# Optimization experiments

Hardware: AMD Instinct MI355X
Metric: run time of the kernel (lower is better)

## Reference

```python
import jax, jax.numpy as jnp
import numpy as np
from jax import lax

THETA = 1.0      # neuron['theta']
TAU_SR = 10.0    # neuron['tauSr'] (SRM synaptic time constant)
TAU_RHO = 1.0    # surrogate-gradient width
SCALE_RHO = 1.0  # surrogate-gradient scale
T_SIM = 100      # simulation['tSample']


def srm_kernel(T, dtype=jnp.float32):
    t = jnp.arange(T, dtype=dtype)
    return (t / TAU_SR) * jnp.exp(1.0 - t / TAU_SR)  # eps(0)=0, peak 1 at t=tau


def psp(x, eps):
    """Causal temporal filter along last axis: y[t] = sum_k eps[k] * x[t-k]."""
    shape = x.shape
    T = shape[-1]
    xf = x.reshape(-1, 1, T)
    k = eps[::-1].reshape(1, 1, T)
    y = lax.conv_general_dilated(xf, k, (1,), [(T - 1, 0)],
                                 dimension_numbers=('NCH', 'OIH', 'NCH'))
    return y.reshape(shape)


def spike(u):
    return (u >= THETA).astype(u.dtype)


def conv_t(x, w, pad):
    """Per-timestep 2D conv. x:[B,C,H,W,T], w:[O,I,kh,kw] -> [B,O,H',W',T]."""
    B, C, H, W, T = x.shape
    xt = jnp.moveaxis(x, -1, 1).reshape(B * T, C, H, W)
    y = lax.conv_general_dilated(xt, w, (1, 1), [(pad, pad), (pad, pad)],
                                 dimension_numbers=('NCHW', 'OIHW', 'NCHW'))
    O, Ho, Wo = y.shape[1], y.shape[2], y.shape[3]
    return jnp.moveaxis(y.reshape(B, T, O, Ho, Wo), 1, -1)


def pool2(x):
    """SLAYER pool: 2x2 sum with fixed weight 1.1. x:[B,C,H,W,T]."""
    B, C, H, W, T = x.shape
    xr = x.reshape(B, C, H // 2, 2, W // 2, 2, T)
    return 1.1 * xr.sum(axis=(3, 5))


def dense_t(x, w):
    """x:[B,C,H,W,T] flattened over CHW; w:[O, C*H*W] -> [B,O,T]."""
    B = x.shape[0]
    T = x.shape[-1]
    xf = x.reshape(B, -1, T)
    return jnp.einsum('bit,oi->bot', xf, w)


def setup_inputs() -> dict:
    key = jax.random.key(0)
    k = jax.random.split(key, 6)
    img = jax.random.uniform(k[0], (32, 1, 28, 28), dtype=jnp.float32)
    rand_u = jax.random.uniform(k[1], (32, 1, 28, 28, T_SIM), dtype=jnp.float32)
    w1 = jax.random.normal(k[2], (16, 1, 5, 5), dtype=jnp.float32) * 0.2
    w2 = jax.random.normal(k[3], (32, 16, 5, 5), dtype=jnp.float32) * 0.05
    wf1 = jax.random.normal(k[4], (410, 1568), dtype=jnp.float32) * 0.05
    wf2 = jax.random.normal(k[5], (10, 410), dtype=jnp.float32) * 0.05
    return {"img": img, "rand_u": rand_u, "w1": w1, "w2": w2, "wf1": wf1, "wf2": wf2}


def reference(img, rand_u, w1, w2, wf1, wf2):
    eps = srm_kernel(T_SIM, img.dtype)
    # rate encoding: Bernoulli spikes with p = pixel intensity
    x = (rand_u < img[..., None]).astype(img.dtype)          # [B,1,28,28,T]
    x = spike(psp(conv_t(x, w1, 2), eps))                    # [B,16,28,28,T]
    x = spike(psp(pool2(x), eps))                            # [B,16,14,14,T]
    x = spike(psp(conv_t(x, w2, 2), eps))                    # [B,32,14,14,T]
    x = spike(psp(pool2(x), eps))                            # [B,32,7,7,T]
    x = spike(psp(dense_t(x, wf1), eps))                     # [B,410,T]
    x = spike(psp(jnp.einsum('bit,oi->bot', x, wf2), eps))   # [B,10,T]
    return x
```

## Files before the change

### kernel.cpp

```cpp
#include <hip/hip_runtime.h>


namespace {
constexpr int B = 32, T = 100;
constexpr double A1 = 0.90483741803595957;
constexpr double CE = 0.27182818284590452;
constexpr double SC39 = 549755813888.0;
constexpr double INV39 = 1.0 / 549755813888.0;

constexpr size_t OFF_M1 = 0;
constexpr size_t OFF_M2 = OFF_M1 + (size_t)B * T * 28 * 4;
constexpr size_t OFF_S4 = OFF_M2 + (size_t)B * T * 224 * 4;
constexpr size_t OFF_D5 = OFF_S4 + (size_t)B * T * 1568;
constexpr size_t OFF_S5 = OFF_D5 + (size_t)B * T * 410 * 8;
constexpr size_t OFF_D6 = OFF_S5 + (size_t)B * T * 410;
constexpr size_t OFF_BP = OFF_D6 + (size_t)B * T * 10 * 8;
constexpr size_t OFF_AP = OFF_D5;
}

using i32x4 = __attribute__((ext_vector_type(4))) int;
using i32x16 = __attribute__((ext_vector_type(16))) int;

__global__ void k_encode_pack(const float* __restrict__ img, const float* __restrict__ ru,
                              unsigned int* __restrict__ m1) {
  int i = blockIdx.x * 256 + threadIdx.x;
  if (i >= B * 28 * T) return;
  int t = i % T;
  int y = (i / T) % 28;
  int b = i / (T * 28);
  unsigned int m = 0;
  const float* rb = ru + ((size_t)b * 784 + y * 28) * T + t;
  const float* ib = img + b * 784 + y * 28;
  for (int x = 0; x < 28; x++) {
    m |= (rb[(size_t)x * T] < ib[x]) ? (1u << x) : 0u;
  }
  m1[((size_t)b * T + t) * 28 + y] = m;
}

__global__ __launch_bounds__(256) void k_conv1(const unsigned int* __restrict__ m1,
                                               const float* __restrict__ w1,
                                               unsigned int* __restrict__ m2) {
  __shared__ double lut[160];
  __shared__ unsigned int mrow[2][32];
  __shared__ unsigned char spk[784];
  __shared__ unsigned char spkP[2][196];
  int o = blockIdx.x % 16, b = blockIdx.x / 16;
  int tid = threadIdx.x;
  if (tid < 160) {
    int dy = tid / 32, f = tid % 32;
    double v = 0.0;
    const float* wb = w1 + o * 25 + dy * 5;
#pragma unroll
    for (int dx = 0; dx < 5; dx++)
      if ((f >> dx) & 1) v += (double)wb[dx];
    lut[tid] = v;
  }
  if (tid < 32) {
    mrow[0][tid] = 0;
    mrow[1][tid] = 0;
  }
  int y = tid / 7, xg = tid % 7;
  int py = tid / 14, px = tid % 14;
  bool act = tid < 196;
  double g1[4] = {0, 0, 0, 0}, g2[4] = {0, 0, 0, 0};
  double p1 = 0.0, p2 = 0.0;
  const unsigned int* m1b = m1 + (size_t)b * T * 28;
  if (tid < 28) mrow[0][tid + 2] = m1b[tid] << 2;
  __syncthreads();
  for (int t = 0; t < T; t++) {
    int cur = t & 1, nxt = cur ^ 1;
    bool dold = (tid < 28) && (t + 1 < T);
    unsigned int ldv = 0;
    if (dold) ldv = m1b[(t + 1) * 28 + tid] << 2;
    if (act) {
      double s0 = 0, s1 = 0, s2 = 0, s3 = 0;
      int xb = xg * 4;
      const unsigned int* mc = mrow[cur];
#pragma unroll
      for (int dy = 0; dy < 5; dy++) {
        unsigned int m = mc[y + dy];
        const double* ld = lut + dy * 32;
        s0 += ld[(m >> (xb + 0)) & 31];
        s1 += ld[(m >> (xb + 1)) & 31];
        s2 += ld[(m >> (xb + 2)) & 31];
        s3 += ld[(m >> (xb + 3)) & 31];
      }
      g1[0] = s0 + A1 * g1[0]; g2[0] = g1[0] + A1 * g2[0];
      g1[1] = s1 + A1 * g1[1]; g2[1] = g1[1] + A1 * g2[1];
      g1[2] = s2 + A1 * g1[2]; g2[2] = g1[2] + A1 * g2[2];
      g1[3] = s3 + A1 * g1[3]; g2[3] = g1[3] + A1 * g2[3];
      unsigned char* sp = spk + y * 28 + xb;
      sp[0] = (CE * (g2[0] - g1[0]) >= 1.0) ? 1 : 0;
      sp[1] = (CE * (g2[1] - g1[1]) >= 1.0) ? 1 : 0;
      sp[2] = (CE * (g2[2] - g1[2]) >= 1.0) ? 1 : 0;
      sp[3] = (CE * (g2[3] - g1[3]) >= 1.0) ? 1 : 0;
    }
    if (dold) mrow[nxt][tid + 2] = ldv;
    __syncthreads();
    if (act) {
      const unsigned char* r0 = spk + (2 * py) * 28 + 2 * px;
      int sum = (int)r0[0] + (int)r0[1] + (int)r0[28] + (int)r0[29];
      double s = 1.1 * (double)sum;
      p1 = s + A1 * p1;
      p2 = p1 + A1 * p2;
      spkP[cur][tid] = (CE * (p2 - p1) >= 1.0) ? 1 : 0;
    }
    if (tid < 14 && t > 0) {
      unsigned int m = 0;
      const unsigned char* rp = spkP[nxt] + tid * 14;
#pragma unroll
      for (int xx = 0; xx < 14; xx++) m |= ((unsigned int)rp[xx]) << xx;
      m2[((size_t)(b * T + (t - 1)) * 16 + o) * 14 + tid] = m;
    }
    __syncthreads();
  }
  if (tid < 14) {
    unsigned int m = 0;
    const unsigned char* rp = spkP[(T - 1) & 1] + tid * 14;
#pragma unroll
    for (int xx = 0; xx < 14; xx++) m |= ((unsigned int)rp[xx]) << xx;
    m2[((size_t)(b * T + (T - 1)) * 16 + o) * 14 + tid] = m;
  }
}

__global__ void k_limbs(const float* __restrict__ w2, signed char* __restrict__ AP) {
  int i = blockIdx.x * 256 + threadIdx.x;
  if (i >= 32 * 80 * 8) return;
  int dx = i & 7;
  int g = (i >> 3) % 80;
  int o = i / 640;
  int c = g >> 2, r = g & 3, eh = r >> 1, kh = r & 1;
  int lane = kh * 32 + o, e = eh * 8 + dx;
  int ci = g / 5, dy = g % 5;
  float wv = (dx < 5) ? w2[((o * 16 + ci) * 5 + dy) * 5 + dx] : 0.0f;
  long long m = llrint((double)wv * SC39);
#pragma unroll
  for (int j = 0; j < 5; j++) {
    int d = (int)((m + 128) & 255) - 128;
    AP[(size_t)((j * 20 + c) * 64 + lane) * 16 + e] = (signed char)d;
    m = (m - d) >> 8;
  }
}

__global__ __launch_bounds__(256, 1) void k_conv2t(const unsigned int* __restrict__ m2,
                                                   const signed char* __restrict__ AP,
                                                   unsigned char* __restrict__ s4) {
  __shared__ unsigned int maskW[2][2][176];
  __shared__ double part[2][2][32][30];
  __shared__ unsigned char spk[2][32][28];
  int yp = blockIdx.x % 7, b = blockIdx.x / 7;
  int y0 = yp * 2;
  int tid = threadIdx.x;
  int w = tid >> 6, l = tid & 63;
  int tp = w >> 1, kg = w & 1;
  int col = l & 31, kh = l >> 5;
  int x = col % 14;
  unsigned int wmask = (col < 28) ? 31u : 0u;
  int half = (col >= 14) ? 1 : 0;
  const unsigned int* m2b = m2 + (size_t)b * T * 224;

  const i32x4* APv = (const i32x4*)AP;
  i32x4 Af[5][10];
#pragma unroll
  for (int j = 0; j < 5; j++)
#pragma unroll
    for (int cl = 0; cl < 10; cl++)
      Af[j][cl] = APv[(size_t)((j * 20) + kg * 10 + cl) * 64 + l];

  double cg1[4] = {0, 0, 0, 0}, cg2[4] = {0, 0, 0, 0};
  double q1 = 0.0, q2 = 0.0;
  int to = tid / 7, pg = tid % 7;
  bool chainAct = tid < 224;

  auto stage = [&](int buf, int baseT) {
    if (w < 2) {
      int tS = baseT + w;
#pragma unroll
      for (int pass = 0; pass < 3; pass++) {
        if (pass == 2 && l >= 32) break;
        int e = pass * 64 + l;
        int H = e / 80, g = e % 80;
        int ci = g / 5, dy = g % 5;
        int iy = y0 - 2 + H + dy;
        unsigned int v = 0;
        if (iy >= 0 && iy < 14 && tS < T) v = m2b[(size_t)tS * 224 + ci * 14 + iy] << 2;
        maskW[buf][w][H * 80 + (g & 1) * 40 + 2 * (g >> 2) + ((g >> 1) & 1)] = v;
      }
    }
  };

  stage(0, 0);
  __syncthreads();

  for (int grp = 0; grp < 50; grp++) {
    int cur = grp & 1, nxt = cur ^ 1;

    {
      const uint4* mwv = (const uint4*)&maskW[cur][tp][0];
      int base4 = half * 20 + kh * 10 + 5 * kg;
      uint4 mk0 = mwv[base4 + 0], mk1 = mwv[base4 + 1], mk2 = mwv[base4 + 2];
      uint4 mk3 = mwv[base4 + 3], mk4 = mwv[base4 + 4];
      i32x16 ac0, ac1, ac2, ac3, ac4;
#pragma unroll
      for (int r = 0; r < 16; r++) { ac0[r] = 0; ac1[r] = 0; ac2[r] = 0; ac3[r] = 0; ac4[r] = 0; }
#pragma unroll
      for (int cl = 0; cl < 10; cl++) {
        uint4 mkv = (cl < 2) ? mk0 : (cl < 4) ? mk1 : (cl < 6) ? mk2 : (cl < 8) ? mk3 : mk4;
        unsigned int ra = (cl & 1) ? mkv.z : mkv.x;
        unsigned int rb = (cl & 1) ? mkv.w : mkv.y;
        unsigned int a5 = (ra >> x) & wmask;
        unsigned int b5 = (rb >> x) & wmask;
        i32x4 bb;
        bb[0] = (int)(((a5 & 15u) * 0x204081u) & 0x01010101u);
        bb[1] = (int)((a5 >> 4) & 1u);
        bb[2] = (int)(((b5 & 15u) * 0x204081u) & 0x01010101u);
        bb[3] = (int)((b5 >> 4) & 1u);
        ac0 = __builtin_amdgcn_mfma_i32_32x32x32_i8(Af[0][cl], bb, ac0, 0, 0, 0);
        ac1 = __builtin_amdgcn_mfma_i32_32x32x32_i8(Af[1][cl], bb, ac1, 0, 0, 0);
        ac2 = __builtin_amdgcn_mfma_i32_32x32x32_i8(Af[2][cl], bb, ac2, 0, 0, 0);
        ac3 = __builtin_amdgcn_mfma_i32_32x32x32_i8(Af[3][cl], bb, ac3, 0, 0, 0);
        ac4 = __builtin_amdgcn_mfma_i32_32x32x32_i8(Af[4][cl], bb, ac4, 0, 0, 0);
      }
      if (col < 28) {
#pragma unroll
        for (int r = 0; r < 16; r++) {
          int R = (r & 3) + 8 * (r >> 2) + 4 * kh;
          int c01 = ac1[r] * 256 + ac0[r];
          int c23 = ac3[r] * 256 + ac2[r];
          double S = ((double)ac4[r] * 65536.0 + (double)c23) * 65536.0 + (double)c01;
          part[tp][kg][R][col] = S;
        }
      }
    }

    stage(nxt, (grp + 1) * 2);
    __syncthreads();

    if (chainAct) {
#pragma unroll
      for (int g = 0; g < 2; g++) {
        const double* pa = &part[g][0][to][pg * 4];
        const double* pb = &part[g][1][to][pg * 4];
        double s0 = (pa[0] + pb[0]) * INV39;
        double s1 = (pa[1] + pb[1]) * INV39;
        double s2 = (pa[2] + pb[2]) * INV39;
        double s3 = (pa[3] + pb[3]) * INV39;
        cg1[0] = s0 + A1 * cg1[0]; cg2[0] = cg1[0] + A1 * cg2[0];
        cg1[1] = s1 + A1 * cg1[1]; cg2[1] = cg1[1] + A1 * cg2[1];
        cg1[2] = s2 + A1 * cg1[2]; cg2[2] = cg1[2] + A1 * cg2[2];
        cg1[3] = s3 + A1 * cg1[3]; cg2[3] = cg1[3] + A1 * cg2[3];
        unsigned int pk = (CE * (cg2[0] - cg1[0]) >= 1.0 ? 1u : 0u)
                        | ((CE * (cg2[1] - cg1[1]) >= 1.0 ? 1u : 0u) << 8)
                        | ((CE * (cg2[2] - cg1[2]) >= 1.0 ? 1u : 0u) << 16)
                        | ((CE * (cg2[3] - cg1[3]) >= 1.0 ? 1u : 0u) << 24);
        *(unsigned int*)&spk[g][to][pg * 4] = pk;
      }
    }
    __syncthreads();

    if (chainAct) {
      int po = to, pp = pg;
#pragma unroll
      for (int g = 0; g < 2; g++) {
        const unsigned char* sr = &spk[g][po][0];
        int sum = (int)sr[2 * pp] + (int)sr[2 * pp + 1] + (int)sr[14 + 2 * pp] + (int)sr[15 + 2 * pp];
        double s = 1.1 * (double)sum;
        q1 = s + A1 * q1;
        q2 = q1 + A1 * q2;
        s4[(size_t)(b * T + grp * 2 + g) * 1568 + po * 49 + yp * 7 + pp] =
            (CE * (q2 - q1) >= 1.0) ? 1 : 0;
      }
    }
  }
}

__global__ void k_limbs2(const float* __restrict__ wf1, signed char* __restrict__ BP) {
  int i = blockIdx.x * 256 + threadIdx.x;
  if (i >= 13 * 5 * 49 * 64) return;
  int lane = i & 63;
  int fi = i >> 6;
  int c = fi % 49;
  int j = (fi / 49) % 5;
  int ot = fi / 245;
  int o = ot * 32 + (lane & 31);
  int kb = 32 * c + (lane >> 5) * 16;
  int wd[4] = {0, 0, 0, 0};
#pragma unroll
  for (int e = 0; e < 16; e++) {
    float wv = (o < 410) ? wf1[(size_t)o * 1568 + kb + e] : 0.0f;
    long long m = llrint((double)wv * SC39);
    int d = 0;
    for (int jj = 0; jj <= j; jj++) {
      d = (int)((m + 128) & 255) - 128;
      m = (m - d) >> 8;
    }
    wd[e >> 2] |= (d & 255) << ((e & 3) * 8);
  }
  i32x4 v;
  v[0] = wd[0]; v[1] = wd[1]; v[2] = wd[2]; v[3] = wd[3];
  *(i32x4*)(BP + (size_t)i * 16) = v;
}

__global__ __launch_bounds__(256) void k_dense1m(const unsigned char* __restrict__ s4,
                                                 const signed char* __restrict__ BP,
                                                 double* __restrict__ d5) {
  int ot = blockIdx.y;
  int w = threadIdx.x >> 6, l = threadIdx.x & 63;
  int col = l & 31, kh = l >> 5;
  int btTile = blockIdx.x * 4 + w;
  const unsigned char* arow = s4 + (size_t)(btTile * 32 + col) * 1568 + kh * 16;
  const i32x4* bpv = (const i32x4*)BP + (size_t)ot * 245 * 64 + l;
  i32x16 acc0, acc1, acc2, acc3, acc4;
#pragma unroll
  for (int r = 0; r < 16; r++) {
    acc0[r] = 0; acc1[r] = 0; acc2[r] = 0; acc3[r] = 0; acc4[r] = 0;
  }
  for (int c = 0; c < 49; c++) {
    i32x4 a = *(const i32x4*)(arow + 32 * c);
    i32x4 b0 = bpv[(0 * 49 + c) * 64];
    i32x4 b1 = bpv[(1 * 49 + c) * 64];
    i32x4 b2 = bpv[(2 * 49 + c) * 64];
    i32x4 b3 = bpv[(3 * 49 + c) * 64];
    i32x4 b4 = bpv[(4 * 49 + c) * 64];
    acc0 = __builtin_amdgcn_mfma_i32_32x32x32_i8(a, b0, acc0, 0, 0, 0);
    acc1 = __builtin_amdgcn_mfma_i32_32x32x32_i8(a, b1, acc1, 0, 0, 0);
    acc2 = __builtin_amdgcn_mfma_i32_32x32x32_i8(a, b2, acc2, 0, 0, 0);
    acc3 = __builtin_amdgcn_mfma_i32_32x32x32_i8(a, b3, acc3, 0, 0, 0);
    acc4 = __builtin_amdgcn_mfma_i32_32x32x32_i8(a, b4, acc4, 0, 0, 0);
  }
  int o = ot * 32 + col;
  if (o < 410) {
#pragma unroll
    for (int r = 0; r < 16; r++) {
      int R = (r & 3) + 8 * (r >> 2) + 4 * kh;
      double v = ((((double)acc4[r] * 256.0 + (double)acc3[r]) * 256.0 +
                   (double)acc2[r]) * 256.0 + (double)acc1[r]) * 256.0 + (double)acc0[r];
      d5[(size_t)(btTile * 32 + R) * 410 + o] = v * INV39;
    }
  }
}

__global__ void k_psp5(const double* __restrict__ d5, unsigned char* __restrict__ s5) {
  int tid = blockIdx.x * 256 + threadIdx.x;
  if (tid >= B * 410) return;
  int o = tid % 410, b = tid / 410;
  double g1 = 0.0, g2 = 0.0;
  for (int t = 0; t < T; t++) {
    double s = d5[(size_t)(b * T + t) * 410 + o];
    g1 = s + A1 * g1;
    g2 = g1 + A1 * g2;
    s5[(size_t)(b * T + t) * 410 + o] = (CE * (g2 - g1) >= 1.0) ? 1 : 0;
  }
}

__global__ void k_dense2(const unsigned char* __restrict__ s5, const float* __restrict__ wf2,
                         double* __restrict__ d6) {
  int tid = blockIdx.x * 256 + threadIdx.x;
  if (tid >= B * T * 10) return;
  int o = tid % 10, bt = tid / 10;
  const unsigned char* sr = s5 + (size_t)bt * 410;
  const float* wr = wf2 + o * 410;
  double s = 0.0;
  for (int i = 0; i < 410; i++) s += (double)wr[i] * (double)sr[i];
  d6[tid] = s;
}

__global__ void k_psp6(const double* __restrict__ d6, float* __restrict__ out) {
  int tid = blockIdx.x * 256 + threadIdx.x;
  if (tid >= B * 10) return;
  int o = tid % 10, b = tid / 10;
  double g1 = 0.0, g2 = 0.0;
  for (int t = 0; t < T; t++) {
    double s = d6[(size_t)(b * T + t) * 10 + o];
    g1 = s + A1 * g1;
    g2 = g1 + A1 * g2;
    out[(size_t)b * 1000 + o * 100 + t] = (CE * (g2 - g1) >= 1.0) ? 1.0f : 0.0f;
  }
}

extern "C" void kernel_launch(void* const* d_in, const int* in_sizes, int n_in,
                              void* d_out, int out_size, void* d_ws, size_t ws_size,
                              hipStream_t stream) {
  const float* img = (const float*)d_in[0];
  const float* ru = (const float*)d_in[1];
  const float* w1 = (const float*)d_in[2];
  const float* w2 = (const float*)d_in[3];
  const float* wf1 = (const float*)d_in[4];
  const float* wf2 = (const float*)d_in[5];

  unsigned char* ws = (unsigned char*)d_ws;
  unsigned int* m1 = (unsigned int*)(ws + OFF_M1);
  unsigned int* m2 = (unsigned int*)(ws + OFF_M2);
  unsigned char* s4 = ws + OFF_S4;
  double* d5 = (double*)(ws + OFF_D5);
  unsigned char* s5 = ws + OFF_S5;
  double* d6 = (double*)(ws + OFF_D6);
  signed char* AP = (signed char*)(ws + OFF_AP);
  signed char* BP = (signed char*)(ws + OFF_BP);
  float* out = (float*)d_out;

  k_encode_pack<<<(B * 28 * T + 255) / 256, 256, 0, stream>>>(img, ru, m1);
  k_limbs<<<(32 * 80 * 8 + 255) / 256, 256, 0, stream>>>(w2, AP);
  k_limbs2<<<(13 * 5 * 49 * 64 + 255) / 256, 256, 0, stream>>>(wf1, BP);
  k_conv1<<<B * 16, 256, 0, stream>>>(m1, w1, m2);
  k_conv2t<<<B * 7, 256, 0, stream>>>(m2, AP, s4);
  k_dense1m<<<dim3(25, 13), 256, 0, stream>>>(s4, BP, d5);
  k_psp5<<<(B * 410 + 255) / 256, 256, 0, stream>>>(d5, s5);
  k_dense2<<<(B * T * 10 + 255) / 256, 256, 0, stream>>>(s5, wf2, d6);
  k_psp6<<<2, 256, 0, stream>>>(d6, out);
}
```

Measured before the change: 412.6 us.

## Remove per-step barrier in conv2 by fusing pooling into PSP chain

Each chain thread now owns the four conv outputs that feed one pooled neuron, so the pool sum is taken in registers and the spike staging buffer and its extra barrier go away. The partial-sum buffer is double-buffered so the next MFMA phase can write without racing the chain readers. The staging addresses are precomputed once, and the next timestep's global loads are issued before the MFMA work so their latency is hidden. In exchange, each chain thread reads strided part entries and shared memory use for the double-buffered partials grows.

```diff
diff --git a/kernel.cpp b/kernel.cpp
--- a/kernel.cpp
+++ b/kernel.cpp
@@ -142,12 +142,11 @@
   }
 }
 
-__global__ __launch_bounds__(256, 1) void k_conv2t(const unsigned int* __restrict__ m2,
+__global__ __launch_bounds__(256, 1) void k_conv2u(const unsigned int* __restrict__ m2,
                                                    const signed char* __restrict__ AP,
                                                    unsigned char* __restrict__ s4) {
   __shared__ unsigned int maskW[2][2][176];
-  __shared__ double part[2][2][32][30];
-  __shared__ unsigned char spk[2][32][28];
+  __shared__ double part[2][2][2][32][30];
   int yp = blockIdx.x % 7, b = blockIdx.x / 7;
   int y0 = yp * 2;
   int tid = threadIdx.x;
@@ -167,36 +166,50 @@
     for (int cl = 0; cl < 10; cl++)
       Af[j][cl] = APv[(size_t)((j * 20) + kg * 10 + cl) * 64 + l];
 
-  double cg1[4] = {0, 0, 0, 0}, cg2[4] = {0, 0, 0, 0};
+  int stPos[3] = {-1, -1, -1}, stIdx[3] = {-1, -1, -1};
+  if (w < 2) {
+#pragma unroll
+    for (int pass = 0; pass < 3; pass++) {
+      if (pass == 2 && l >= 32) continue;
+      int e = pass * 64 + l;
+      int H = e / 80, g = e % 80;
+      int ci = g / 5, dy = g % 5;
+      int iy = y0 - 2 + H + dy;
+      stPos[pass] = H * 80 + (g & 1) * 40 + 2 * (g >> 2) + ((g >> 1) & 1);
+      if (iy >= 0 && iy < 14) stIdx[pass] = ci * 14 + iy;
+    }
+  }
+
+  int po = tid / 7, pp = tid % 7;
+  bool chainAct = tid < 224;
+  double sg1[4] = {0, 0, 0, 0}, sg2[4] = {0, 0, 0, 0};
   double q1 = 0.0, q2 = 0.0;
-  int to = tid / 7, pg = tid % 7;
-  bool chainAct = tid < 224;
-
-  auto stage = [&](int buf, int baseT) {
-    if (w < 2) {
-      int tS = baseT + w;
-#pragma unroll
-      for (int pass = 0; pass < 3; pass++) {
-        if (pass == 2 && l >= 32) break;
-        int e = pass * 64 + l;
-        int H = e / 80, g = e % 80;
-        int ci = g / 5, dy = g % 5;
-        int iy = y0 - 2 + H + dy;
-        unsigned int v = 0;
-        if (iy >= 0 && iy < 14 && tS < T) v = m2b[(size_t)tS * 224 + ci * 14 + iy] << 2;
-        maskW[buf][w][H * 80 + (g & 1) * 40 + 2 * (g >> 2) + ((g >> 1) & 1)] = v;
-      }
-    }
-  };
-
-  stage(0, 0);
+
+  if (w < 2) {
+#pragma unroll
+    for (int pass = 0; pass < 3; pass++) {
+      if (stPos[pass] < 0) continue;
+      unsigned int v = 0;
+      if (stIdx[pass] >= 0) v = m2b[(size_t)w * 224 + stIdx[pass]] << 2;
+      maskW[0][w][stPos[pass]] = v;
+    }
+  }
   __syncthreads();
 
   for (int grp = 0; grp < 50; grp++) {
-    int cur = grp & 1, nxt = cur ^ 1;
+    int p = grp & 1, np = p ^ 1;
+
+    unsigned int ld0 = 0, ld1 = 0, ld2 = 0;
+    bool doStage = (w < 2) && (grp + 1 < 50);
+    if (doStage) {
+      size_t tb = (size_t)((grp + 1) * 2 + w) * 224;
+      if (stIdx[0] >= 0) ld0 = m2b[tb + stIdx[0]] << 2;
+      if (stIdx[1] >= 0) ld1 = m2b[tb + stIdx[1]] << 2;
+      if (stIdx[2] >= 0) ld2 = m2b[tb + stIdx[2]] << 2;
+    }
 
     {
-      const uint4* mwv = (const uint4*)&maskW[cur][tp][0];
+      const uint4* mwv = (const uint4*)&maskW[p][tp][0];
       int base4 = half * 20 + kh * 10 + 5 * kg;
       uint4 mk0 = mwv[base4 + 0], mk1 = mwv[base4 + 1], mk2 = mwv[base4 + 2];
       uint4 mk3 = mwv[base4 + 3], mk4 = mwv[base4 + 4];
@@ -228,42 +241,37 @@
           int c01 = ac1[r] * 256 + ac0[r];
           int c23 = ac3[r] * 256 + ac2[r];
           double S = ((double)ac4[r] * 65536.0 + (double)c23) * 65536.0 + (double)c01;
-          part[tp][kg][R][col] = S;
+          part[p][tp][kg][R][col] = S;
         }
       }
     }
 
-    stage(nxt, (grp + 1) * 2);
+    if (doStage) {
+      if (stPos[0] >= 0) maskW[np][w][stPos[0]] = ld0;
+      if (stPos[1] >= 0) maskW[np][w][stPos[1]] = ld1;
+      if (stPos[2] >= 0) maskW[np][w][stPos[2]] = ld2;
+    }
     __syncthreads();
 
     if (chainAct) {
 #pragma unroll
       for (int g = 0; g < 2; g++) {
-        const double* pa = &part[g][0][to][pg * 4];
-        const double* pb = &part[g][1][to][pg * 4];
-        double s0 = (pa[0] + pb[0]) * INV39;
-        double s1 = (pa[1] + pb[1]) * INV39;
-        double s2 = (pa[2] + pb[2]) * INV39;
-        double s3 = (pa[3] + pb[3]) * INV39;
-        cg1[0] = s0 + A1 * cg1[0]; cg2[0] = cg1[0] + A1 * cg2[0];
-        cg1[1] = s1 + A1 * cg1[1]; cg2[1] = cg1[1] + A1 * cg2[1];
-        cg1[2] = s2 + A1 * cg1[2]; cg2[2] = cg1[2] + A1 * cg2[2];
-        cg1[3] = s3 + A1 * cg1[3]; cg2[3] = cg1[3] + A1 * cg2[3];
-        unsigned int pk = (CE * (cg2[0] - cg1[0]) >= 1.0 ? 1u : 0u)
-                        | ((CE * (cg2[1] - cg1[1]) >= 1.0 ? 1u : 0u) << 8)
-                        | ((CE * (cg2[2] - cg1[2]) >= 1.0 ? 1u : 0u) << 16)
-                        | ((CE * (cg2[3] - cg1[3]) >= 1.0 ? 1u : 0u) << 24);
-        *(unsigned int*)&spk[g][to][pg * 4] = pk;
-      }
-    }
-    __syncthreads();
-
-    if (chainAct) {
-      int po = to, pp = pg;
-#pragma unroll
-      for (int g = 0; g < 2; g++) {
-        const unsigned char* sr = &spk[g][po][0];
-        int sum = (int)sr[2 * pp] + (int)sr[2 * pp + 1] + (int)sr[14 + 2 * pp] + (int)sr[15 + 2 * pp];
+        const double* a0 = &part[p][g][0][po][2 * pp];
+        const double* b0 = &part[p][g][1][po][2 * pp];
+        const double* a1 = &part[p][g][0][po][14 + 2 * pp];
+        const double* b1 = &part[p][g][1][po][14 + 2 * pp];
+        double c0 = (a0[0] + b0[0]) * INV39;
+        double c1 = (a0[1] + b0[1]) * INV39;
+        double c2 = (a1[0] + b1[0]) * INV39;
+        double c3 = (a1[1] + b1[1]) * INV39;
+        sg1[0] = c0 + A1 * sg1[0]; sg2[0] = sg1[0] + A1 * sg2[0];
+        sg1[1] = c1 + A1 * sg1[1]; sg2[1] = sg1[1] + A1 * sg2[1];
+        sg1[2] = c2 + A1 * sg1[2]; sg2[2] = sg1[2] + A1 * sg2[2];
+        sg1[3] = c3 + A1 * sg1[3]; sg2[3] = sg1[3] + A1 * sg2[3];
+        int sum = ((CE * (sg2[0] - sg1[0]) >= 1.0) ? 1 : 0)
+                + ((CE * (sg2[1] - sg1[1]) >= 1.0) ? 1 : 0)
+                + ((CE * (sg2[2] - sg1[2]) >= 1.0) ? 1 : 0)
+                + ((CE * (sg2[3] - sg1[3]) >= 1.0) ? 1 : 0);
         double s = 1.1 * (double)sum;
         q1 = s + A1 * q1;
         q2 = q1 + A1 * q2;
@@ -403,7 +411,7 @@
   k_limbs<<<(32 * 80 * 8 + 255) / 256, 256, 0, stream>>>(w2, AP);
   k_limbs2<<<(13 * 5 * 49 * 64 + 255) / 256, 256, 0, stream>>>(wf1, BP);
   k_conv1<<<B * 16, 256, 0, stream>>>(m1, w1, m2);
-  k_conv2t<<<B * 7, 256, 0, stream>>>(m2, AP, s4);
+  k_conv2u<<<B * 7, 256, 0, stream>>>(m2, AP, s4);
   k_dense1m<<<dim3(25, 13), 256, 0, stream>>>(s4, BP, d5);
   k_psp5<<<(B * 410 + 255) / 256, 256, 0, stream>>>(d5, s5);
   k_dense2<<<(B * T * 10 + 255) / 256, 256, 0, stream>>>(s5, wf2, d6);
```

Measured after the change: 404.8 us. Within noise of the previous version (-1.9%).
